# Performance work log

Hardware: AMD Instinct MI355X
Metric: run time of the kernel (lower is better)

## Reference

```python
import jax, jax.numpy as jnp
import numpy as np

B, K, H, W = 8, 4, 256, 256
HID = 16
DT, STEPS, JITERS, OMEGA = 0.1, 12, 8, 0.9
D_MAX, CHI_MAX, K_MAX = 2.0, 2.0, 1.0


def _conv2d(x, w, b):
    y = jax.lax.conv_general_dilated(x, w, (1, 1), 'SAME',
                                     dimension_numbers=('NCHW', 'OIHW', 'NCHW'))
    return y + b[None, :, None, None]


def _pad(x):  # replicate pad by 1 on H, W
    return jnp.pad(x, ((0, 0), (0, 0), (1, 1), (1, 1)), mode='edge')


def laplacian(x):
    xp = _pad(x)
    return (xp[:, :, :-2, 1:-1] + xp[:, :, 2:, 1:-1]
            + xp[:, :, 1:-1, :-2] + xp[:, :, 1:-1, 2:] - 4.0 * x)


def gradient(x):
    xp = _pad(x)
    gx = xp[:, :, 1:-1, 2:] - x   # forward diff along W
    gy = xp[:, :, 2:, 1:-1] - x   # forward diff along H
    return gx, gy


def divergence(vx, vy):
    xp = _pad(vx)
    yp = _pad(vy)
    dvx = vx - xp[:, :, 1:-1, 2:]
    dvy = vy - yp[:, :, 2:, 1:-1]
    return dvx + dvy


def project_simplex(p, eps=1e-8):
    # p: [..., K]; faithful port incl. the rho-1 indexing of the torch code
    Kc = p.shape[-1]
    x = jnp.nan_to_num(p)
    u = jnp.flip(jnp.sort(x, axis=-1), axis=-1)            # descending
    cssv = jnp.cumsum(u, axis=-1) - 1.0
    ind = jnp.arange(1, Kc + 1, dtype=x.dtype)
    cond = (u - cssv / ind) > 0
    rho = jnp.argmax(cond.astype(jnp.int32) * jnp.arange(1, Kc + 1), axis=-1)
    rho_idx = jnp.maximum(rho - 1, 0)[..., None]
    tau = jnp.take_along_axis(cssv, rho_idx, axis=-1) / jnp.maximum(rho_idx + 1, 1)
    tau = jnp.nan_to_num(tau)
    w = jnp.maximum(x - tau, 0.0)
    return w / (w.sum(-1, keepdims=True) + eps)


def setup_inputs() -> dict:
    key = jax.random.key(0)
    ks = jax.random.split(key, 8)
    p0 = jax.random.uniform(ks[0], (B, K, H, W), dtype=jnp.float32)
    p0 = p0 / p0.sum(1, keepdims=True)
    w1 = jax.random.normal(ks[1], (HID, K, 3, 3), jnp.float32) * np.sqrt(2.0 / (K * 9))
    w2 = jax.random.normal(ks[2], (HID, HID, 3, 3), jnp.float32) * np.sqrt(2.0 / (HID * 9))
    w3 = jax.random.normal(ks[3], (1, HID, 1, 1), jnp.float32) * np.sqrt(1.0 / HID)
    return {
        'p0': p0,
        'D_raw': jnp.full((K,), 0.5, jnp.float32),
        'chi_raw': jnp.float32(0.5),
        'k_tumor_raw': jnp.float32(0.3),
        'cap_tumor_logit': jnp.float32(np.log(0.7) - np.log(0.3)),
        'w1': w1, 'b1': jnp.zeros((HID,), jnp.float32),
        'w2': w2, 'b2': jnp.zeros((HID,), jnp.float32),
        'w3': w3, 'b3': jnp.zeros((1,), jnp.float32),
        'tumor_idx': 0,
    }


def _forward(p0, D_raw, chi_raw, k_tumor_raw, cap_tumor_logit,
             w1, b1, w2, b2, w3, b3, tumor_idx):
    ti = int(tumor_idx)
    sp = jax.nn.softplus
    D_all = jnp.minimum(sp(D_raw) + 1e-8, D_MAX)                 # [K]
    chi = jnp.minimum(sp(chi_raw) + 1e-8, CHI_MAX)
    k_t = jnp.minimum(sp(k_tumor_raw) + 1e-8, K_MAX)             # unused in tumor_map mode
    cap_t = jnp.clip(jax.nn.sigmoid(cap_tumor_logit), 0.001, 0.95)

    # GrowthCNN (k_mode='tumor_map')
    h = jax.nn.relu(_conv2d(p0, w1, b1))
    h = jax.nn.relu(_conv2d(h, w2, b2))
    k_map = jnp.maximum(jax.nn.sigmoid(_conv2d(h, w3, b3)) * K_MAX, 1e-6)  # [B,1,H,W]

    D4 = D_all[None, :, None, None]
    diag = 1.0 + DT * D4 * 4.0

    p = jnp.maximum(jnp.nan_to_num(p0), 0.0)
    for _ in range(STEPS):
        gx, gy = gradient(p)
        gx = jnp.nan_to_num(gx)
        gy = jnp.nan_to_num(gy)
        sum_gx = gx.sum(1, keepdims=True)
        sum_gy = gy.sum(1, keepdims=True)
        fx = jnp.nan_to_num(-chi * p * (sum_gx - gx))
        fy = jnp.nan_to_num(-chi * p * (sum_gy - gy))
        cross = jnp.nan_to_num(divergence(fx, fy))

        pt = jnp.clip(p[:, ti:ti + 1], 0.0, 1.0)
        rt = jnp.nan_to_num(k_map * pt * (1.0 - pt / cap_t))
        react = jnp.zeros_like(p).at[:, ti:ti + 1].set(rt)

        rhs = jnp.nan_to_num(p + DT * (cross + react))

        # damped Jacobi for implicit diffusion, vectorized over channels
        xk = p
        for _it in range(JITERS):
            Lx = laplacian(xk)
            r = rhs - (xk - DT * D4 * Lx)
            xk = jnp.nan_to_num(xk + (OMEGA / diag) * r)

        p = project_simplex(jnp.moveaxis(xk, 1, -1))
        p = jnp.maximum(jnp.nan_to_num(jnp.moveaxis(p, -1, 1)), 0.0)
    return p


def reference(p0, D_raw, chi_raw, k_tumor_raw, cap_tumor_logit,
              w1, b1, w2, b2, w3, b3, tumor_idx):
    return _forward(p0, D_raw, chi_raw, k_tumor_raw, cap_tumor_logit,
                    w1, b1, w2, b2, w3, b3, tumor_idx)


if __name__ == '__main__':
    out = reference(**setup_inputs())
    print(out.shape, out.dtype)
```

## Files before the change

kernel.cpp:

```cpp
#include <hip/hip_runtime.h>
#include <math.h>

#define B_ 8
#define K4 4
#define H_ 256
#define W_ 256
#define HID_ 16
#define DT_ 0.1f
#define STEPS_ 12
#define OMEGA_ 0.9f
#define D_MAX_ 2.0f
#define CHI_MAX_ 2.0f
#define HW_ (H_ * W_)

__device__ __forceinline__ int clampi(int v, int lo, int hi) { return min(max(v, lo), hi); }

__device__ __forceinline__ float softplus_f(float x) {
    return fmaxf(x, 0.0f) + log1pf(expf(-fabsf(x)));
}

__device__ __forceinline__ void proj4(float v0, float v1, float v2, float v3,
                                      float& o0, float& o1, float& o2, float& o3) {
    float u0 = v0, u1 = v1, u2 = v2, u3 = v3, t;
    t = fmaxf(u0, u1); u1 = fminf(u0, u1); u0 = t;
    t = fmaxf(u2, u3); u3 = fminf(u2, u3); u2 = t;
    t = fmaxf(u0, u2); u2 = fminf(u0, u2); u0 = t;
    t = fmaxf(u1, u3); u3 = fminf(u1, u3); u1 = t;
    t = fmaxf(u1, u2); u2 = fminf(u1, u2); u1 = t;
    float cs1 = u0 + u1;
    float cs2 = cs1 + u2;
    float c0 = u0 - 1.0f;
    float c1 = cs1 - 1.0f;
    float c2 = cs2 - 1.0f;
    int rho = 0;
    if (u1 - c1 / 2.0f > 0.0f) rho = 1;
    if (u2 - c2 / 3.0f > 0.0f) rho = 2;
    if (u3 - (cs2 + u3 - 1.0f) / 4.0f > 0.0f) rho = 3;
    int ri = rho - 1; if (ri < 0) ri = 0;
    float tau = (ri == 0) ? c0 : (ri == 1) ? (c1 / 2.0f) : (c2 / 3.0f);
    float w0 = fmaxf(v0 - tau, 0.0f);
    float w1 = fmaxf(v1 - tau, 0.0f);
    float w2 = fmaxf(v2 - tau, 0.0f);
    float w3 = fmaxf(v3 - tau, 0.0f);
    float inv = 1.0f / (w0 + w1 + w2 + w3 + 1e-8f);
    o0 = w0 * inv; o1 = w1 * inv; o2 = w2 * inv; o3 = w3 * inv;
}

__global__ void setup_kernel(const float* __restrict__ D_raw,
                             const float* __restrict__ chi_raw,
                             const float* __restrict__ cap_logit,
                             const float* __restrict__ w1,
                             const float* __restrict__ w2,
                             float* __restrict__ params,
                             float* __restrict__ w1t,
                             float* __restrict__ w2t) {
    int tid = threadIdx.x;
    if (tid == 0) {
        for (int c = 0; c < K4; ++c) {
            float d = fminf(softplus_f(D_raw[c]) + 1e-8f, D_MAX_);
            params[c]      = d;
            params[6 + c]  = DT_ * d;
            params[10 + c] = OMEGA_ / (1.0f + DT_ * d * 4.0f);
        }
        params[4] = fminf(softplus_f(chi_raw[0]) + 1e-8f, CHI_MAX_);
        float ct = 1.0f / (1.0f + expf(-cap_logit[0]));
        params[5] = fminf(fmaxf(ct, 0.001f), 0.95f);
    }
    for (int i = tid; i < 576; i += 256) {
        int o = i & 15, rest = i >> 4, ic = rest / 9, k = rest % 9;
        w1t[i] = w1[(o * K4 + ic) * 9 + k];
    }
    for (int i = tid; i < 2304; i += 256) {
        int o = i & 15, rest = i >> 4, ic = rest / 9, k = rest % 9;
        w2t[i] = w2[(o * HID_ + ic) * 9 + k];
    }
}

#define PS2_(c,ry,rx) csmem[((c)*20 + (ry))*24 + (rx)]
#define HS2_(o,ry,rx) csmem[1920 + ((o)*18 + (ry))*21 + (rx)]
#define PSUM_ (1920 + 6048)

__global__ __launch_bounds__(512) void cnn_kernel(const float* __restrict__ p0,
                                                  const float* __restrict__ w1t,
                                                  const float* __restrict__ b1,
                                                  const float* __restrict__ w2t,
                                                  const float* __restrict__ b2,
                                                  const float* __restrict__ w3,
                                                  const float* __restrict__ b3,
                                                  float* __restrict__ kmap) {
    __shared__ float csmem[1920 + 6048 + 512];
    const int tid = threadIdx.x;
    const int tx0 = blockIdx.x * 16, ty0 = blockIdx.y * 16, b = blockIdx.z;

    for (int i = tid; i < 4 * 20 * 20; i += 512) {
        int c = i / 400, r = i % 400;
        int ry = r / 20, rx = r % 20;
        int gy = ty0 + ry - 2, gx = tx0 + rx - 2;
        float v = 0.0f;
        if ((unsigned)gy < 256u && (unsigned)gx < 256u)
            v = p0[(((size_t)b * K4 + c) << 16) + gy * W_ + gx];
        PS2_(c, ry, rx) = v;
    }
    __syncthreads();

    if (tid < 18 * 18) {
        int iy = tid / 18, ixx = tid % 18;
        int gy = ty0 + iy - 1, gx = tx0 + ixx - 1;
        bool indom = ((unsigned)gy < 256u) && ((unsigned)gx < 256u);
        float acc[HID_];
#pragma unroll
        for (int o = 0; o < HID_; ++o) acc[o] = b1[o];
        for (int ic = 0; ic < K4; ++ic)
            for (int ky = 0; ky < 3; ++ky)
#pragma unroll
                for (int kx = 0; kx < 3; ++kx) {
                    float v = PS2_(ic, iy + ky, ixx + kx);
                    const float* wp = w1t + (ic * 9 + ky * 3 + kx) * 16;
#pragma unroll
                    for (int o = 0; o < HID_; ++o)
                        acc[o] = fmaf(wp[o], v, acc[o]);
                }
#pragma unroll
        for (int o = 0; o < HID_; ++o)
            HS2_(o, iy, ixx) = indom ? fmaxf(acc[o], 0.0f) : 0.0f;
    }
    __syncthreads();

    {
        int px = tid & 255;
        int hb = __builtin_amdgcn_readfirstlane((tid >> 8) & 1) * 8;
        int iy2 = px >> 4, ix2 = px & 15;
        float acc[8];
#pragma unroll
        for (int o = 0; o < 8; ++o) acc[o] = b2[hb + o];
        for (int ic = 0; ic < HID_; ++ic)
            for (int ky = 0; ky < 3; ++ky)
#pragma unroll
                for (int kx = 0; kx < 3; ++kx) {
                    float v = HS2_(ic, iy2 + ky, ix2 + kx);
                    const float* wp = w2t + (ic * 9 + ky * 3 + kx) * 16 + hb;
#pragma unroll
                    for (int o = 0; o < 8; ++o)
                        acc[o] = fmaf(wp[o], v, acc[o]);
                }
        float s = 0.0f;
#pragma unroll
        for (int o = 0; o < 8; ++o)
            s += w3[hb + o] * fmaxf(acc[o], 0.0f);
        csmem[PSUM_ + (tid >> 8) * 256 + px] = s;
    }
    __syncthreads();

    if (tid < 256) {
        int iy2 = tid >> 4, ix2 = tid & 15;
        float s = b3[0] + csmem[PSUM_ + tid] + csmem[PSUM_ + 256 + tid];
        float km = 1.0f / (1.0f + expf(-s));
        km = fmaxf(km, 1e-6f);
        kmap[((size_t)b << 16) + (ty0 + iy2) * W_ + tx0 + ix2] = km;
    }
}

#define PP_(c,ry,rx) psm[((c)*18 + (ry))*20 + (rx)]

__global__ __launch_bounds__(256) void proj_rhs_kernel(const float* __restrict__ xin,
                                                       const float* __restrict__ kmap,
                                                       const float* __restrict__ params,
                                                       const int* __restrict__ tumor_idx,
                                                       float* __restrict__ pout,
                                                       float* __restrict__ rhs,
                                                       int mode) {
    const int tid = threadIdx.x;
    const int tx0 = blockIdx.x * 16, ty0 = blockIdx.y * 16, b = blockIdx.z;

    if (mode == 2) {
        int ry = tid >> 4, rx = tid & 15;
        size_t off = ((size_t)(b * K4) << 16) + (ty0 + ry) * W_ + tx0 + rx;
        float v0 = xin[off];
        float v1 = xin[off + HW_];
        float v2 = xin[off + 2 * HW_];
        float v3 = xin[off + 3 * HW_];
        proj4(v0, v1, v2, v3, v0, v1, v2, v3);
        pout[off]           = v0;
        pout[off + HW_]     = v1;
        pout[off + 2 * HW_] = v2;
        pout[off + 3 * HW_] = v3;
        return;
    }

    __shared__ float psm[4 * 18 * 20];

    for (int i = tid; i < 18 * 18; i += 256) {
        int ry = i / 18, rx = i % 18;
        int gy = clampi(ty0 + ry, 0, 255);
        int gx = clampi(tx0 + rx, 0, 255);
        size_t off = (((size_t)b * K4) << 16) + gy * W_ + gx;
        float v0 = xin[off], v1 = xin[off + HW_];
        float v2 = xin[off + 2 * HW_], v3 = xin[off + 3 * HW_];
        if (mode == 0) {
            v0 = fmaxf(v0, 0.0f); v1 = fmaxf(v1, 0.0f);
            v2 = fmaxf(v2, 0.0f); v3 = fmaxf(v3, 0.0f);
        } else {
            proj4(v0, v1, v2, v3, v0, v1, v2, v3);
        }
        PP_(0, ry, rx) = v0; PP_(1, ry, rx) = v1;
        PP_(2, ry, rx) = v2; PP_(3, ry, rx) = v3;
    }
    __syncthreads();

    const float chi = params[4], cap = params[5];
    const int ti = tumor_idx[0];
    int ry = tid >> 4, rx = tid & 15;
    int gy = ty0 + ry, gx = tx0 + rx;
    int row1 = clampi(gy + 1, 0, 255) - ty0;
    int row2 = clampi(gy + 2, 0, 255) - ty0;
    int col1 = clampi(gx + 1, 0, 255) - tx0;
    int col2 = clampi(gx + 2, 0, 255) - tx0;
    float pc[4], px1[4], py1[4], g0x[4], g1x[4], g0y[4], g1y[4];
    float s0x = 0.f, s1x = 0.f, s0y = 0.f, s1y = 0.f;
#pragma unroll
    for (int c = 0; c < 4; ++c) {
        float pcv = PP_(c, ry, rx);
        float a   = PP_(c, ry, col1);
        float bb  = PP_(c, ry, col2);
        float d   = PP_(c, row1, rx);
        float e   = PP_(c, row2, rx);
        pc[c] = pcv; px1[c] = a; py1[c] = d;
        g0x[c] = a - pcv;  g1x[c] = bb - a;
        g0y[c] = d - pcv;  g1y[c] = e - d;
        s0x += g0x[c]; s1x += g1x[c]; s0y += g0y[c]; s1y += g1y[c];
    }
    float km = kmap[((size_t)b << 16) + gy * W_ + gx];
    size_t off = (((size_t)b * K4) << 16) + gy * W_ + gx;
#pragma unroll
    for (int c = 0; c < 4; ++c) {
        float fx0 = -chi * pc[c]  * (s0x - g0x[c]);
        float fx1 = -chi * px1[c] * (s1x - g1x[c]);
        float fy0 = -chi * pc[c]  * (s0y - g0y[c]);
        float fy1 = -chi * py1[c] * (s1y - g1y[c]);
        float cross = (fx0 - fx1) + (fy0 - fy1);
        float react = 0.0f;
        if (c == ti) {
            float pt = fminf(fmaxf(pc[c], 0.0f), 1.0f);
            react = km * pt * (1.0f - pt / cap);
        }
        rhs[off + (size_t)c * HW_]  = pc[c] + DT_ * (cross + react);
        pout[off + (size_t)c * HW_] = pc[c];
    }
}

#define JROWS 82
#define JSTR 88
#define JX_(buf,row,col) jsm[(buf)*(JROWS*JSTR) + (row)*JSTR + (col)]

__device__ __forceinline__ float4 jac_core(float4 up, float4 dn, float lf, float rt,
                                           float4 ce, float4 rsv,
                                           bool lm, bool rm, float dtD, float wod) {
    float l0 = lm ? ce.x : lf;
    float r3 = rm ? ce.w : rt;
    float4 ov;
    {
        float lap = up.x + dn.x + l0 + ce.y - 4.0f * ce.x;
        float r = rsv.x - (ce.x - dtD * lap);
        ov.x = ce.x + wod * r;
    }
    {
        float lap = up.y + dn.y + ce.x + ce.z - 4.0f * ce.y;
        float r = rsv.y - (ce.y - dtD * lap);
        ov.y = ce.y + wod * r;
    }
    {
        float lap = up.z + dn.z + ce.y + ce.w - 4.0f * ce.z;
        float r = rsv.z - (ce.z - dtD * lap);
        ov.z = ce.z + wod * r;
    }
    {
        float lap = up.w + dn.w + ce.z + r3 - 4.0f * ce.w;
        float r = rsv.w - (ce.w - dtD * lap);
        ov.w = ce.w + wod * r;
    }
    return ov;
}

__global__ __launch_bounds__(1024, 8) void jacobi8_kernel(const float* __restrict__ p,
                                                          const float* __restrict__ rhs,
                                                          const float* __restrict__ params,
                                                          float* __restrict__ xk) {
    __shared__ float jsm[2 * JROWS * JSTR];
    const int tid = threadIdx.x;
    const int lane = tid & 63;
    const int tx0 = blockIdx.x * 64, ty0 = blockIdx.y * 64;
    const int bc = blockIdx.z;
    const int c  = bc & 3;
    const float* pc_ = p + ((size_t)bc << 16);

    for (int i = tid; i < 80 * 80; i += 1024) {
        int r = i / 80, x = i % 80;
        int gy = clampi(ty0 + r - 8, 0, 255);
        int gx = clampi(tx0 + x - 8, 0, 255);
        JX_(0, r + 1, x + 4) = pc_[gy * W_ + gx];
    }

    const float dtD = params[6 + c];
    const float wod = params[10 + c];
    const float* rbase = rhs + ((size_t)bc << 16);

    const int ryA = tid / 20, gA = tid % 20;
    const int gyA = ty0 + ryA - 8;
    const int gx0A = tx0 + 4 * gA - 8;
    const int ycA = ryA + 1;
    const int yuA = clampi(gyA - 1, 0, 255) - ty0 + 9;
    const int ydA = clampi(gyA + 1, 0, 255) - ty0 + 9;
    const int ixA = 4 + 4 * gA;
    const bool lmA = (gx0A == 0), rmA = (gx0A == 252);
    const bool lfFixA = (lane == 0 && gA > 0);
    const bool rtFixA = (lane == 63 && gA < 19);

    const bool hasB = (tid < 576);
    const int itB = tid + 1024;
    const int ryB = itB / 20, gB = itB % 20;
    const int gyB = ty0 + ryB - 8;
    const int gx0B = tx0 + 4 * gB - 8;
    const int ycB = ryB + 1;
    const int yuB = clampi(gyB - 1, 0, 255) - ty0 + 9;
    const int ydB = clampi(gyB + 1, 0, 255) - ty0 + 9;
    const int ixB = 4 + 4 * gB;
    const bool lmB = (gx0B == 0), rmB = (gx0B == 252);
    const bool lfFixB = (lane == 0 && gB > 0);
    const bool rtFixB = (lane == 63 && gB < 19);

    float4 rsvA, rsvB;
    {
        const float* rr = rbase + clampi(gyA, 0, 255) * W_;
        if (gx0A >= 0 && gx0A <= 252) {
            rsvA = *(const float4*)&rr[gx0A];
        } else {
            rsvA.x = rr[clampi(gx0A,     0, 255)];
            rsvA.y = rr[clampi(gx0A + 1, 0, 255)];
            rsvA.z = rr[clampi(gx0A + 2, 0, 255)];
            rsvA.w = rr[clampi(gx0A + 3, 0, 255)];
        }
    }
    if (hasB) {
        const float* rr = rbase + clampi(gyB, 0, 255) * W_;
        if (gx0B >= 0 && gx0B <= 252) {
            rsvB = *(const float4*)&rr[gx0B];
        } else {
            rsvB.x = rr[clampi(gx0B,     0, 255)];
            rsvB.y = rr[clampi(gx0B + 1, 0, 255)];
            rsvB.z = rr[clampi(gx0B + 2, 0, 255)];
            rsvB.w = rr[clampi(gx0B + 3, 0, 255)];
        }
    }
    __syncthreads();

    float4 ceA = *(const float4*)&JX_(0, ycA, ixA);
    float4 ceB;
    if (hasB) ceB = *(const float4*)&JX_(0, ycB, ixB);

#pragma unroll
    for (int j = 0; j < 8; ++j) {
        const int rb = j & 1;
        const float* rp = &jsm[rb * (JROWS * JSTR)];
        float* wpb = &jsm[(rb ^ 1) * (JROWS * JSTR)];

        float lfA = __shfl_up(ceA.w, 1);
        float rtA = __shfl_down(ceA.x, 1);
        if (lfFixA) lfA = rp[ycA * JSTR + ixA - 1];
        if (rtFixA) rtA = rp[ycA * JSTR + ixA + 4];
        float4 upA = *(const float4*)&rp[yuA * JSTR + ixA];
        float4 dnA = *(const float4*)&rp[ydA * JSTR + ixA];
        float4 ovA = jac_core(upA, dnA, lfA, rtA, ceA, rsvA, lmA, rmA, dtD, wod);

        float4 ovB;
        if (hasB) {
            float lfB = __shfl_up(ceB.w, 1);
            float rtB = __shfl_down(ceB.x, 1);
            if (lfFixB) lfB = rp[ycB * JSTR + ixB - 1];
            if (rtFixB) rtB = rp[ycB * JSTR + ixB + 4];
            float4 upB = *(const float4*)&rp[yuB * JSTR + ixB];
            float4 dnB = *(const float4*)&rp[ydB * JSTR + ixB];
            ovB = jac_core(upB, dnB, lfB, rtB, ceB, rsvB, lmB, rmB, dtD, wod);
        }

        if (j < 7) {
            *(float4*)&wpb[ycA * JSTR + ixA] = ovA;
            if (hasB) *(float4*)&wpb[ycB * JSTR + ixB] = ovB;
            __syncthreads();
        }
        ceA = ovA;
        if (hasB) ceB = ovB;
    }

    if (ryA >= 8 && ryA < 72 && gA >= 2 && gA < 18)
        *(float4*)&xk[((size_t)bc << 16) + gyA * W_ + gx0A] = ceA;
    if (hasB && ryB >= 8 && ryB < 72 && gB >= 2 && gB < 18)
        *(float4*)&xk[((size_t)bc << 16) + gyB * W_ + gx0B] = ceB;
}

extern "C" void kernel_launch(void* const* d_in, const int* in_sizes, int n_in,
                              void* d_out, int out_size, void* d_ws, size_t ws_size,
                              hipStream_t stream) {
    const float* p0        = (const float*)d_in[0];
    const float* D_raw     = (const float*)d_in[1];
    const float* chi_raw   = (const float*)d_in[2];
    const float* cap_logit = (const float*)d_in[4];
    const float* w1        = (const float*)d_in[5];
    const float* b1        = (const float*)d_in[6];
    const float* w2        = (const float*)d_in[7];
    const float* b2        = (const float*)d_in[8];
    const float* w3        = (const float*)d_in[9];
    const float* b3        = (const float*)d_in[10];
    const int*   tumor_idx = (const int*)d_in[11];

    char* ws = (char*)d_ws;
    float* params = (float*)(ws + 0);
    float* w1t    = (float*)(ws + 1024);
    float* w2t    = (float*)(ws + 4096);
    float* kmap   = (float*)(ws + 65536);
    float* p      = (float*)(ws + 4  * 1024 * 1024);
    float* rhs    = (float*)(ws + 12 * 1024 * 1024);
    float* xk     = (float*)d_out;

    setup_kernel<<<1, 256, 0, stream>>>(D_raw, chi_raw, cap_logit, w1, w2,
                                        params, w1t, w2t);
    dim3 cgrid(16, 16, B_);
    cnn_kernel<<<cgrid, 512, 0, stream>>>(p0, w1t, b1, w2t, b2, w3, b3, kmap);

    dim3 pgrid(16, 16, B_);
    dim3 jgrid(4, 4, B_ * K4);
    for (int s = 0; s < STEPS_; ++s) {
        const float* xin = (s == 0) ? p0 : xk;
        proj_rhs_kernel<<<pgrid, 256, 0, stream>>>(xin, kmap, params, tumor_idx,
                                                   p, rhs, s == 0 ? 0 : 1);
        jacobi8_kernel<<<jgrid, 1024, 0, stream>>>(p, rhs, params, xk);
    }
    proj_rhs_kernel<<<pgrid, 256, 0, stream>>>(xk, kmap, params, tumor_idx,
                                               xk, rhs, 2);
}
```

Measured before the change: 359.9 us.

## Fuse all time steps into one cooperative persistent kernel with grid syncs

Replaces the 24 per-step launches of the projection/RHS and Jacobi kernels with one cooperative kernel of 256 blocks of 1024 threads. Each block handles eight RHS tiles, then two channel planes of Jacobi work, separated by grid.sync(). The final projection is done in the same kernel. The aim is to remove launch overhead and inter-kernel gaps, at the cost of grid-wide barriers and fewer resident blocks (256 blocks, two Jacobi planes processed serially per block). The original launch sequence remains as a fallback if the cooperative launch fails.

```diff
diff --git a/kernel.cpp b/kernel.cpp
--- a/kernel.cpp
+++ b/kernel.cpp
@@ -1,5 +1,8 @@
 #include <hip/hip_runtime.h>
+#include <hip/hip_cooperative_groups.h>
 #include <math.h>
+
+namespace cg = cooperative_groups;
 
 #define B_ 8
 #define K4 4
@@ -160,6 +163,258 @@
     }
 }
 
+#define JROWS 82
+#define JSTR 88
+#define JTOT (JROWS * JSTR)
+
+__device__ __forceinline__ float4 jac_core(float4 up, float4 dn, float lf, float rt,
+                                           float4 ce, float4 rsv,
+                                           bool lm, bool rm, float dtD, float wod) {
+    float l0 = lm ? ce.x : lf;
+    float r3 = rm ? ce.w : rt;
+    float4 ov;
+    {
+        float lap = up.x + dn.x + l0 + ce.y - 4.0f * ce.x;
+        float r = rsv.x - (ce.x - dtD * lap);
+        ov.x = ce.x + wod * r;
+    }
+    {
+        float lap = up.y + dn.y + ce.x + ce.z - 4.0f * ce.y;
+        float r = rsv.y - (ce.y - dtD * lap);
+        ov.y = ce.y + wod * r;
+    }
+    {
+        float lap = up.z + dn.z + ce.y + ce.w - 4.0f * ce.z;
+        float r = rsv.z - (ce.z - dtD * lap);
+        ov.z = ce.z + wod * r;
+    }
+    {
+        float lap = up.w + dn.w + ce.z + r3 - 4.0f * ce.w;
+        float r = rsv.w - (ce.w - dtD * lap);
+        ov.w = ce.w + wod * r;
+    }
+    return ov;
+}
+
+__global__ __launch_bounds__(1024, 4) void coop_steps(const float* __restrict__ p0,
+                                                      const float* __restrict__ kmap,
+                                                      const float* __restrict__ params,
+                                                      const int* __restrict__ tumor_idx,
+                                                      float* __restrict__ p,
+                                                      float* __restrict__ rhs,
+                                                      float* __restrict__ xk) {
+    cg::grid_group grid = cg::this_grid();
+    __shared__ float jsm[2 * JTOT];
+
+    const int tid = threadIdx.x;
+    const int lane = tid & 63;
+    const int L = (blockIdx.z * 4 + blockIdx.y) * 4 + blockIdx.x;
+
+    const int g4 = tid >> 8;
+    const int px = tid & 255;
+    float* ppg = &jsm[g4 * 1472];
+#define PPG_(c,ry,rx) ppg[((c)*18 + (ry))*20 + (rx)]
+
+    const int jtx0 = blockIdx.x * 64, jty0 = blockIdx.y * 64;
+    const int ryA = tid / 20, gA = tid % 20;
+    const int gyA = jty0 + ryA - 8;
+    const int gx0A = jtx0 + 4 * gA - 8;
+    const int ycA = ryA + 1;
+    const int yuA = clampi(gyA - 1, 0, 255) - jty0 + 9;
+    const int ydA = clampi(gyA + 1, 0, 255) - jty0 + 9;
+    const int ixA = 4 + 4 * gA;
+    const bool lmA = (gx0A == 0), rmA = (gx0A == 252);
+    const bool lfFixA = (lane == 0 && gA > 0);
+    const bool rtFixA = (lane == 63 && gA < 19);
+
+    const bool hasB = (tid < 576);
+    const int itB = tid + 1024;
+    const int ryB = itB / 20, gB = itB % 20;
+    const int gyB = jty0 + ryB - 8;
+    const int gx0B = jtx0 + 4 * gB - 8;
+    const int ycB = ryB + 1;
+    const int yuB = clampi(gyB - 1, 0, 255) - jty0 + 9;
+    const int ydB = clampi(gyB + 1, 0, 255) - jty0 + 9;
+    const int ixB = 4 + 4 * gB;
+    const bool lmB = (gx0B == 0), rmB = (gx0B == 252);
+    const bool lfFixB = (lane == 0 && gB > 0);
+    const bool rtFixB = (lane == 63 && gB < 19);
+
+    const float chi = params[4], cap = params[5];
+    const int ti = tumor_idx[0];
+
+    for (int s = 0; s < STEPS_; ++s) {
+        const float* xin = (s == 0) ? p0 : xk;
+        for (int half = 0; half < 2; ++half) {
+            int T = L * 8 + half * 4 + g4;
+            int pb = T >> 8;
+            int pty0 = ((T >> 4) & 15) * 16;
+            int ptx0 = (T & 15) * 16;
+
+            for (int i = px; i < 324; i += 256) {
+                int ry = i / 18, rx = i % 18;
+                int gy = clampi(pty0 + ry, 0, 255);
+                int gx = clampi(ptx0 + rx, 0, 255);
+                size_t off = (((size_t)pb * K4) << 16) + gy * W_ + gx;
+                float v0 = xin[off], v1 = xin[off + HW_];
+                float v2 = xin[off + 2 * HW_], v3 = xin[off + 3 * HW_];
+                if (s == 0) {
+                    v0 = fmaxf(v0, 0.0f); v1 = fmaxf(v1, 0.0f);
+                    v2 = fmaxf(v2, 0.0f); v3 = fmaxf(v3, 0.0f);
+                } else {
+                    proj4(v0, v1, v2, v3, v0, v1, v2, v3);
+                }
+                PPG_(0, ry, rx) = v0; PPG_(1, ry, rx) = v1;
+                PPG_(2, ry, rx) = v2; PPG_(3, ry, rx) = v3;
+            }
+            __syncthreads();
+
+            {
+                int ry = px >> 4, rx = px & 15;
+                int gy = pty0 + ry, gx = ptx0 + rx;
+                int row1 = clampi(gy + 1, 0, 255) - pty0;
+                int row2 = clampi(gy + 2, 0, 255) - pty0;
+                int col1 = clampi(gx + 1, 0, 255) - ptx0;
+                int col2 = clampi(gx + 2, 0, 255) - ptx0;
+                float pc[4], px1[4], py1[4], g0x[4], g1x[4], g0y[4], g1y[4];
+                float s0x = 0.f, s1x = 0.f, s0y = 0.f, s1y = 0.f;
+#pragma unroll
+                for (int c = 0; c < 4; ++c) {
+                    float pcv = PPG_(c, ry, rx);
+                    float a   = PPG_(c, ry, col1);
+                    float bb  = PPG_(c, ry, col2);
+                    float d   = PPG_(c, row1, rx);
+                    float e   = PPG_(c, row2, rx);
+                    pc[c] = pcv; px1[c] = a; py1[c] = d;
+                    g0x[c] = a - pcv;  g1x[c] = bb - a;
+                    g0y[c] = d - pcv;  g1y[c] = e - d;
+                    s0x += g0x[c]; s1x += g1x[c]; s0y += g0y[c]; s1y += g1y[c];
+                }
+                float km = kmap[((size_t)pb << 16) + gy * W_ + gx];
+                size_t off = (((size_t)pb * K4) << 16) + gy * W_ + gx;
+#pragma unroll
+                for (int c = 0; c < 4; ++c) {
+                    float fx0 = -chi * pc[c]  * (s0x - g0x[c]);
+                    float fx1 = -chi * px1[c] * (s1x - g1x[c]);
+                    float fy0 = -chi * pc[c]  * (s0y - g0y[c]);
+                    float fy1 = -chi * py1[c] * (s1y - g1y[c]);
+                    float cross = (fx0 - fx1) + (fy0 - fy1);
+                    float react = 0.0f;
+                    if (c == ti) {
+                        float pt = fminf(fmaxf(pc[c], 0.0f), 1.0f);
+                        react = km * pt * (1.0f - pt / cap);
+                    }
+                    rhs[off + (size_t)c * HW_] = pc[c] + DT_ * (cross + react);
+                    p[off + (size_t)c * HW_]   = pc[c];
+                }
+            }
+            __syncthreads();
+        }
+        grid.sync();
+
+        for (int half = 0; half < 2; ++half) {
+            const int bc = blockIdx.z * 2 + half;
+            const int jc = bc & 3;
+            const float dtD = params[6 + jc];
+            const float wod = params[10 + jc];
+            const float* pc_ = p + ((size_t)bc << 16);
+
+            for (int i = tid; i < 80 * 80; i += 1024) {
+                int r = i / 80, x = i % 80;
+                int gy = clampi(jty0 + r - 8, 0, 255);
+                int gx = clampi(jtx0 + x - 8, 0, 255);
+                jsm[(r + 1) * JSTR + (x + 4)] = pc_[gy * W_ + gx];
+            }
+
+            const float* rbase = rhs + ((size_t)bc << 16);
+            float4 rsvA, rsvB;
+            {
+                const float* rr = rbase + clampi(gyA, 0, 255) * W_;
+                if (gx0A >= 0 && gx0A <= 252) {
+                    rsvA = *(const float4*)&rr[gx0A];
+                } else {
+                    rsvA.x = rr[clampi(gx0A,     0, 255)];
+                    rsvA.y = rr[clampi(gx0A + 1, 0, 255)];
+                    rsvA.z = rr[clampi(gx0A + 2, 0, 255)];
+                    rsvA.w = rr[clampi(gx0A + 3, 0, 255)];
+                }
+            }
+            if (hasB) {
+                const float* rr = rbase + clampi(gyB, 0, 255) * W_;
+                if (gx0B >= 0 && gx0B <= 252) {
+                    rsvB = *(const float4*)&rr[gx0B];
+                } else {
+                    rsvB.x = rr[clampi(gx0B,     0, 255)];
+                    rsvB.y = rr[clampi(gx0B + 1, 0, 255)];
+                    rsvB.z = rr[clampi(gx0B + 2, 0, 255)];
+                    rsvB.w = rr[clampi(gx0B + 3, 0, 255)];
+                }
+            }
+            __syncthreads();
+
+            float4 ceA = *(const float4*)&jsm[ycA * JSTR + ixA];
+            float4 ceB;
+            if (hasB) ceB = *(const float4*)&jsm[ycB * JSTR + ixB];
+
+#pragma unroll
+            for (int j = 0; j < 8; ++j) {
+                const int rb = j & 1;
+                const float* rp = &jsm[rb * JTOT];
+                float* wpb = &jsm[(rb ^ 1) * JTOT];
+
+                float lfA = __shfl_up(ceA.w, 1);
+                float rtA = __shfl_down(ceA.x, 1);
+                if (lfFixA) lfA = rp[ycA * JSTR + ixA - 1];
+                if (rtFixA) rtA = rp[ycA * JSTR + ixA + 4];
+                float4 upA = *(const float4*)&rp[yuA * JSTR + ixA];
+                float4 dnA = *(const float4*)&rp[ydA * JSTR + ixA];
+                float4 ovA = jac_core(upA, dnA, lfA, rtA, ceA, rsvA, lmA, rmA, dtD, wod);
+
+                float4 ovB;
+                if (hasB) {
+                    float lfB = __shfl_up(ceB.w, 1);
+                    float rtB = __shfl_down(ceB.x, 1);
+                    if (lfFixB) lfB = rp[ycB * JSTR + ixB - 1];
+                    if (rtFixB) rtB = rp[ycB * JSTR + ixB + 4];
+                    float4 upB = *(const float4*)&rp[yuB * JSTR + ixB];
+                    float4 dnB = *(const float4*)&rp[ydB * JSTR + ixB];
+                    ovB = jac_core(upB, dnB, lfB, rtB, ceB, rsvB, lmB, rmB, dtD, wod);
+                }
+
+                if (j < 7) {
+                    *(float4*)&wpb[ycA * JSTR + ixA] = ovA;
+                    if (hasB) *(float4*)&wpb[ycB * JSTR + ixB] = ovB;
+                    __syncthreads();
+                }
+                ceA = ovA;
+                if (hasB) ceB = ovB;
+            }
+
+            if (ryA >= 8 && ryA < 72 && gA >= 2 && gA < 18)
+                *(float4*)&xk[((size_t)bc << 16) + gyA * W_ + gx0A] = ceA;
+            if (hasB && ryB >= 8 && ryB < 72 && gB >= 2 && gB < 18)
+                *(float4*)&xk[((size_t)bc << 16) + gyB * W_ + gx0B] = ceB;
+            __syncthreads();
+        }
+        grid.sync();
+    }
+
+    for (int k = 0; k < 2; ++k) {
+        int i = L * 2048 + k * 1024 + tid;
+        int b = i >> 16, ppx = i & 65535;
+        size_t off = (((size_t)b * K4) << 16) + ppx;
+        float v0 = xk[off];
+        float v1 = xk[off + HW_];
+        float v2 = xk[off + 2 * HW_];
+        float v3 = xk[off + 3 * HW_];
+        proj4(v0, v1, v2, v3, v0, v1, v2, v3);
+        xk[off]           = v0;
+        xk[off + HW_]     = v1;
+        xk[off + 2 * HW_] = v2;
+        xk[off + 3 * HW_] = v3;
+    }
+}
+
 #define PP_(c,ry,rx) psm[((c)*18 + (ry))*20 + (rx)]
 
 __global__ __launch_bounds__(256) void proj_rhs_kernel(const float* __restrict__ xin,
@@ -248,44 +503,11 @@
     }
 }
 
-#define JROWS 82
-#define JSTR 88
-#define JX_(buf,row,col) jsm[(buf)*(JROWS*JSTR) + (row)*JSTR + (col)]
-
-__device__ __forceinline__ float4 jac_core(float4 up, float4 dn, float lf, float rt,
-                                           float4 ce, float4 rsv,
-                                           bool lm, bool rm, float dtD, float wod) {
-    float l0 = lm ? ce.x : lf;
-    float r3 = rm ? ce.w : rt;
-    float4 ov;
-    {
-        float lap = up.x + dn.x + l0 + ce.y - 4.0f * ce.x;
-        float r = rsv.x - (ce.x - dtD * lap);
-        ov.x = ce.x + wod * r;
-    }
-    {
-        float lap = up.y + dn.y + ce.x + ce.z - 4.0f * ce.y;
-        float r = rsv.y - (ce.y - dtD * lap);
-        ov.y = ce.y + wod * r;
-    }
-    {
-        float lap = up.z + dn.z + ce.y + ce.w - 4.0f * ce.z;
-        float r = rsv.z - (ce.z - dtD * lap);
-        ov.z = ce.z + wod * r;
-    }
-    {
-        float lap = up.w + dn.w + ce.z + r3 - 4.0f * ce.w;
-        float r = rsv.w - (ce.w - dtD * lap);
-        ov.w = ce.w + wod * r;
-    }
-    return ov;
-}
-
 __global__ __launch_bounds__(1024, 8) void jacobi8_kernel(const float* __restrict__ p,
                                                           const float* __restrict__ rhs,
                                                           const float* __restrict__ params,
                                                           float* __restrict__ xk) {
-    __shared__ float jsm[2 * JROWS * JSTR];
+    __shared__ float jsm[2 * JTOT];
     const int tid = threadIdx.x;
     const int lane = tid & 63;
     const int tx0 = blockIdx.x * 64, ty0 = blockIdx.y * 64;
@@ -297,7 +519,7 @@
         int r = i / 80, x = i % 80;
         int gy = clampi(ty0 + r - 8, 0, 255);
         int gx = clampi(tx0 + x - 8, 0, 255);
-        JX_(0, r + 1, x + 4) = pc_[gy * W_ + gx];
+        jsm[(r + 1) * JSTR + (x + 4)] = pc_[gy * W_ + gx];
     }
 
     const float dtD = params[6 + c];
@@ -353,15 +575,15 @@
     }
     __syncthreads();
 
-    float4 ceA = *(const float4*)&JX_(0, ycA, ixA);
+    float4 ceA = *(const float4*)&jsm[ycA * JSTR + ixA];
     float4 ceB;
-    if (hasB) ceB = *(const float4*)&JX_(0, ycB, ixB);
+    if (hasB) ceB = *(const float4*)&jsm[ycB * JSTR + ixB];
 
 #pragma unroll
     for (int j = 0; j < 8; ++j) {
         const int rb = j & 1;
-        const float* rp = &jsm[rb * (JROWS * JSTR)];
-        float* wpb = &jsm[(rb ^ 1) * (JROWS * JSTR)];
+        const float* rp = &jsm[rb * JTOT];
+        float* wpb = &jsm[(rb ^ 1) * JTOT];
 
         float lfA = __shfl_up(ceA.w, 1);
         float rtA = __shfl_down(ceA.x, 1);
@@ -426,14 +648,22 @@
     dim3 cgrid(16, 16, B_);
     cnn_kernel<<<cgrid, 512, 0, stream>>>(p0, w1t, b1, w2t, b2, w3, b3, kmap);
 
-    dim3 pgrid(16, 16, B_);
-    dim3 jgrid(4, 4, B_ * K4);
-    for (int s = 0; s < STEPS_; ++s) {
-        const float* xin = (s == 0) ? p0 : xk;
-        proj_rhs_kernel<<<pgrid, 256, 0, stream>>>(xin, kmap, params, tumor_idx,
-                                                   p, rhs, s == 0 ? 0 : 1);
-        jacobi8_kernel<<<jgrid, 1024, 0, stream>>>(p, rhs, params, xk);
-    }
-    proj_rhs_kernel<<<pgrid, 256, 0, stream>>>(xk, kmap, params, tumor_idx,
-                                               xk, rhs, 2);
-}
+    void* args[] = {(void*)&p0, (void*)&kmap, (void*)&params, (void*)&tumor_idx,
+                    (void*)&p, (void*)&rhs, (void*)&xk};
+    hipError_t e = hipLaunchCooperativeKernel((const void*)coop_steps,
+                                              dim3(4, 4, 16), dim3(1024),
+                                              args, 0, stream);
+    if (e != hipSuccess) {
+        (void)hipGetLastError();
+        dim3 pgrid(16, 16, B_);
+        dim3 jgrid(4, 4, B_ * K4);
+        for (int s = 0; s < STEPS_; ++s) {
+            const float* xin = (s == 0) ? p0 : xk;
+            proj_rhs_kernel<<<pgrid, 256, 0, stream>>>(xin, kmap, params, tumor_idx,
+                                                       p, rhs, s == 0 ? 0 : 1);
+            jacobi8_kernel<<<jgrid, 1024, 0, stream>>>(p, rhs, params, xk);
+        }
+        proj_rhs_kernel<<<pgrid, 256, 0, stream>>>(xk, kmap, params, tumor_idx,
+                                                   xk, rhs, 2);
+    }
+}
```

After: 1.181 ms. +228.2%, slower.
